# Kernel optimization log

Hardware: AMD Instinct MI355X
Metric: run time of the kernel (lower is better)

## Reference

```python
import jax, jax.numpy as jnp
import numpy as np

N = 50000      # nodes
E = 800000     # edges (before self-loops)
D = 128        # input_dim == hidden_dim
L = 3          # num_layers
EPS = 1e-5     # BatchNorm eps


def setup_inputs() -> dict:
    key = jax.random.key(0)
    k0, k1, k2 = jax.random.split(key, 3)
    x = jax.random.normal(k0, (N, D), dtype=jnp.float32)
    edge_index = jax.random.randint(k1, (2, E), 0, N, dtype=jnp.int32)
    # stacked per-layer params (layer 0 is input_dim->hidden, same shape since D==hidden)
    W = jax.random.normal(k2, (L, D, D), dtype=jnp.float32) / np.float32(np.sqrt(D))
    b = jnp.zeros((L, D), dtype=jnp.float32)
    gamma = jnp.ones((L, D), dtype=jnp.float32)
    beta = jnp.zeros((L, D), dtype=jnp.float32)
    return {"x": x, "edge_index": edge_index, "W": W, "b": b, "gamma": gamma, "beta": beta}


def reference(x, edge_index, W, b, gamma, beta):
    # --- GCN symmetric normalization with self-loops (PyG GCNConv default) ---
    loop = jnp.arange(N, dtype=edge_index.dtype)
    src = jnp.concatenate([edge_index[0], loop])      # [E+N]
    dst = jnp.concatenate([edge_index[1], loop])      # [E+N]
    deg = jax.ops.segment_sum(jnp.ones_like(dst, dtype=x.dtype), dst, num_segments=N)
    dinv = jax.lax.rsqrt(deg)                          # deg >= 1 due to self-loops
    norm = (dinv[src] * dinv[dst])[:, None]            # [E+N, 1]

    h = x
    for i in range(L):
        # GCNConv: aggregate norm * (h W)[src] into dst, then bias
        m = h @ W[i]                                   # [N, D]
        h = jax.ops.segment_sum(m[src] * norm, dst, num_segments=N) + b[i]
        # BatchNorm1d (training-mode batch statistics, biased variance)
        mu = jnp.mean(h, axis=0)
        var = jnp.var(h, axis=0)
        h = gamma[i] * (h - mu) * jax.lax.rsqrt(var + EPS) + beta[i]
        # ReLU; dropout is identity in eval mode
        h = jax.nn.relu(h)
    return h
```

## Files before the change

kernel.cpp:

```cpp
#include <hip/hip_runtime.h>
#include <hip/hip_bf16.h>

#define N_NODES 50000
#define N_EDGES 800000
#define DIM 128
#define BN_EPS 1e-5f
#define GATHER_BLOCKS (N_NODES / 4)
#define RED_BLOCKS 125
#define CAP 48

#define PART_SHIFT 7
#define PART_SIZE 128
#define NPARTS ((N_NODES + PART_SIZE - 1) / PART_SIZE)
#define QSTRIDE 32
#define BIN_EPB 2048
#define BIN_BLOCKS ((N_EDGES + BIN_EPB - 1) / BIN_EPB)
#define QCAP2 2560
#define GEMM_BLOCKS ((N_NODES + 31) / 32)

typedef __attribute__((ext_vector_type(8))) short short8;
typedef __attribute__((ext_vector_type(4))) float float4v;

__device__ __forceinline__ float bf16_bits_to_f32(unsigned short u) {
    union { unsigned int i; float f; } c;
    c.i = ((unsigned int)u) << 16;
    return c.f;
}

__device__ __forceinline__ float bf16_lo(unsigned int u) {
    union { unsigned int i; float f; } c;
    c.i = u << 16;
    return c.f;
}

__device__ __forceinline__ float bf16_hi(unsigned int u) {
    union { unsigned int i; float f; } c;
    c.i = u & 0xFFFF0000u;
    return c.f;
}

__device__ __forceinline__ unsigned short f32_to_bf16_bits(float f) {
    union { float f; unsigned int i; } c;
    c.f = f;
    unsigned int lsb = (c.i >> 16) & 1u;
    c.i += 0x7FFFu + lsb;
    return (unsigned short)(c.i >> 16);
}

__global__ __launch_bounds__(256) void zero_int(int* __restrict__ p, int n) {
    int i = blockIdx.x * blockDim.x + threadIdx.x;
    if (i < n) p[i] = 0;
}

__global__ __launch_bounds__(256) void prep(
    const unsigned short* __restrict__ xu,
    const void* __restrict__ W, const void* __restrict__ b,
    const void* __restrict__ g, const void* __restrict__ be,
    float* __restrict__ modeg, unsigned short* __restrict__ Wt,
    float* __restrict__ pf32,
    int* __restrict__ qcnt, float* __restrict__ stats, int* __restrict__ done) {
    __shared__ int okc;
    if (threadIdx.x == 0) okc = 0;
    __syncthreads();
    int ok = 0;
    for (int i = threadIdx.x; i < 512; i += 256) {
        unsigned e = (xu[i] >> 7) & 0xFFu;
        if (e >= 96u && e <= 159u) ok++;
    }
    atomicAdd(&okc, ok);
    __syncthreads();
    const bool mf32 = okc < 480;

    if (blockIdx.x == 0) {
        if (threadIdx.x == 0) { modeg[0] = mf32 ? 1.0f : 0.0f; done[0] = 0; done[1] = 0; }
        for (int i = threadIdx.x; i < NPARTS; i += 256) qcnt[(size_t)i * QSTRIDE] = 0;
        stats[threadIdx.x] = 0.0f;
    }

    int i = blockIdx.x * 256 + threadIdx.x;
    const int NW = 3 * DIM * DIM;
    if (i < NW) {
        int l = i >> 14;
        int rem = i & 16383;
        int k = rem >> 7;
        int n = rem & 127;
        unsigned short v = mf32 ? f32_to_bf16_bits(((const float*)W)[i])
                                : ((const unsigned short*)W)[i];
        Wt[(size_t)l * DIM * DIM + (size_t)n * DIM + k] = v;
    } else if (i < NW + 3 * 3 * DIM) {
        int p = i - NW;
        int which = p / 384;
        int r = p - which * 384;
        const void* srcp = (which == 0) ? b : (which == 1) ? g : be;
        float v = mf32 ? ((const float*)srcp)[r]
                       : bf16_bits_to_f32(((const unsigned short*)srcp)[r]);
        pf32[which * 384 + r] = v;
    }
}

__global__ __launch_bounds__(256) void fused_a(
    const int* __restrict__ src, const int* __restrict__ dst,
    int* __restrict__ qcnt, unsigned int* __restrict__ queue,
    const void* __restrict__ x, const unsigned short* __restrict__ Wt,
    const float* __restrict__ mode, unsigned short* __restrict__ A) {
    __shared__ int lcnt[NPARTS];
    __shared__ int loff[NPARTS];
    const int bid = blockIdx.x;
    if (bid < BIN_BLOCKS) {
        const int t = threadIdx.x;
        const int blk0 = bid * BIN_EPB;
        const int nval = min(BIN_EPB, N_EDGES - blk0);
        for (int i = t; i < NPARTS; i += 256) lcnt[i] = 0;
        __syncthreads();
        for (int li = t; li < nval; li += 256) {
            int d = dst[blk0 + li];
            if ((unsigned)d < (unsigned)N_NODES)
                atomicAdd(&lcnt[d >> PART_SHIFT], 1);
        }
        __syncthreads();
        for (int i = t; i < NPARTS; i += 256) {
            int c = lcnt[i];
            loff[i] = c ? atomicAdd(&qcnt[(size_t)i * QSTRIDE], c) : 0;
        }
        __syncthreads();
        for (int li = t; li < nval; li += 256) {
            int d = dst[blk0 + li];
            if ((unsigned)d < (unsigned)N_NODES) {
                int s = src[blk0 + li];
                int part = d >> PART_SHIFT;
                int pos = atomicAdd(&loff[part], 1);
                if (pos < QCAP2)
                    queue[(size_t)part * QCAP2 + pos] =
                        (unsigned int)(s & 0xFFFF) |
                        ((unsigned int)(d & (PART_SIZE - 1)) << 16);
            }
        }
        return;
    }
    const int wave = threadIdx.x >> 6;
    const int lane = threadIdx.x & 63;
    const int quad = lane >> 4;
    const int nidx = lane & 15;
    const int row0 = (bid - BIN_BLOCKS) * 32;
    const bool mf = mode[0] > 0.5f;

    short8 bfrag[2][4];
    #pragma unroll
    for (int half = 0; half < 2; ++half) {
        int c = wave * 32 + half * 16 + nidx;
        #pragma unroll
        for (int kk = 0; kk < 4; ++kk)
            bfrag[half][kk] = *(const short8*)(Wt + (size_t)c * DIM + kk * 32 + quad * 8);
    }

    #pragma unroll
    for (int tile = 0; tile < 2; ++tile) {
        const int rt = row0 + tile * 16;
        if (rt >= N_NODES) break;
        short8 afrag[4];
        if (mf) {
            const float* xf = (const float*)x;
            #pragma unroll
            for (int kk = 0; kk < 4; ++kk) {
                const float4v* xr = (const float4v*)(xf + (size_t)(rt + nidx) * DIM + kk * 32 + quad * 8);
                float4v p0 = xr[0], p1 = xr[1];
                #pragma unroll
                for (int j = 0; j < 4; ++j) {
                    afrag[kk][j]     = (short)f32_to_bf16_bits(p0[j]);
                    afrag[kk][4 + j] = (short)f32_to_bf16_bits(p1[j]);
                }
            }
        } else {
            const unsigned short* hu = (const unsigned short*)x;
            #pragma unroll
            for (int kk = 0; kk < 4; ++kk)
                afrag[kk] = *(const short8*)(hu + (size_t)(rt + nidx) * DIM + kk * 32 + quad * 8);
        }

        float4v acc0 = {0.f, 0.f, 0.f, 0.f};
        float4v acc1 = {0.f, 0.f, 0.f, 0.f};
        #pragma unroll
        for (int kk = 0; kk < 4; ++kk) {
            acc0 = __builtin_amdgcn_mfma_f32_16x16x32_bf16(afrag[kk], bfrag[0][kk], acc0, 0, 0, 0);
            acc1 = __builtin_amdgcn_mfma_f32_16x16x32_bf16(afrag[kk], bfrag[1][kk], acc1, 0, 0, 0);
        }

        #pragma unroll
        for (int r = 0; r < 4; ++r) {
            int row = rt + quad * 4 + r;
            size_t i0 = (size_t)row * DIM + wave * 32 + nidx;
            A[i0]      = f32_to_bf16_bits(acc0[r]);
            A[i0 + 16] = f32_to_bf16_bits(acc1[r]);
        }
    }
}

__global__ __launch_bounds__(256) void csr_build(
    const int* __restrict__ qcnt, const unsigned int* __restrict__ queue,
    unsigned short* __restrict__ colu, int* __restrict__ cnt,
    float* __restrict__ dinv) {
    __shared__ int lcnt[PART_SIZE];
    const int p = blockIdx.x;
    if (threadIdx.x < PART_SIZE) lcnt[threadIdx.x] = 0;
    __syncthreads();
    const int base = p << PART_SHIFT;
    const int n = min(qcnt[(size_t)p * QSTRIDE], QCAP2);
    const unsigned int* qp = queue + (size_t)p * QCAP2;
    for (int i = threadIdx.x; i < n; i += 256) {
        unsigned int pk = qp[i];
        int dl = (pk >> 16) & (PART_SIZE - 1);
        int s  = pk & 0xFFFFu;
        int pos = atomicAdd(&lcnt[dl], 1);
        if (pos < CAP)
            colu[(size_t)(base + dl) * CAP + pos] = (unsigned short)s;
    }
    __syncthreads();
    if (threadIdx.x < PART_SIZE) {
        int d = base + threadIdx.x;
        if (d < N_NODES) {
            int c = lcnt[threadIdx.x];
            cnt[d] = c;
            dinv[d] = rsqrtf((float)c + 1.0f);
        }
    }
}

__global__ __launch_bounds__(256) void make_dinv(const int* __restrict__ cnt,
                                                 float* __restrict__ dinv) {
    int v = blockIdx.x * blockDim.x + threadIdx.x;
    if (v < N_NODES) dinv[v] = rsqrtf((float)cnt[v] + 1.0f);
}

__global__ __launch_bounds__(256) void gemm_scale(
    const void* hsrc, int kind, int b_bf16,
    const unsigned short* __restrict__ Wt,
    const float* __restrict__ dinv,
    const float* __restrict__ mode,
    const float* __restrict__ alpha, const float* __restrict__ delta,
    unsigned short* A, float* __restrict__ B, int write_b) {
    const int wave = threadIdx.x >> 6;
    const int lane = threadIdx.x & 63;
    const int quad = lane >> 4;
    const int nidx = lane & 15;
    const int row0 = blockIdx.x * 32;
    const bool mf = mode[0] > 0.5f;

    short8 bfrag[2][4];
    #pragma unroll
    for (int half = 0; half < 2; ++half) {
        int c = wave * 32 + half * 16 + nidx;
        #pragma unroll
        for (int kk = 0; kk < 4; ++kk)
            bfrag[half][kk] = *(const short8*)(Wt + (size_t)c * DIM + kk * 32 + quad * 8);
    }

    #pragma unroll
    for (int tile = 0; tile < 2; ++tile) {
        const int rt = row0 + tile * 16;
        if (rt >= N_NODES) break;

        short8 afrag[4];
        if (kind == 0) {
            if (mf) {
                const float* xf = (const float*)hsrc;
                #pragma unroll
                for (int kk = 0; kk < 4; ++kk) {
                    const float4v* xr = (const float4v*)(xf + (size_t)(rt + nidx) * DIM + kk * 32 + quad * 8);
                    float4v p0 = xr[0], p1 = xr[1];
                    #pragma unroll
                    for (int j = 0; j < 4; ++j) {
                        afrag[kk][j]     = (short)f32_to_bf16_bits(p0[j]);
                        afrag[kk][4 + j] = (short)f32_to_bf16_bits(p1[j]);
                    }
                }
            } else {
                const unsigned short* hu = (const unsigned short*)hsrc;
                #pragma unroll
                for (int kk = 0; kk < 4; ++kk)
                    afrag[kk] = *(const short8*)(hu + (size_t)(rt + nidx) * DIM + kk * 32 + quad * 8);
            }
        } else if (b_bf16) {
            const unsigned short* Bh = (const unsigned short*)hsrc;
            const float dv = dinv[rt + nidx];
            #pragma unroll
            for (int kk = 0; kk < 4; ++kk) {
                short8 braw = *(const short8*)(Bh + (size_t)(rt + nidx) * DIM + kk * 32 + quad * 8);
                const float* ap = alpha + kk * 32 + quad * 8;
                const float* dp = delta + kk * 32 + quad * 8;
                float4v A0 = *(const float4v*)ap, A1 = *(const float4v*)(ap + 4);
                float4v D0 = *(const float4v*)dp, D1 = *(const float4v*)(dp + 4);
                #pragma unroll
                for (int j = 0; j < 4; ++j) {
                    float v0 = bf16_bits_to_f32((unsigned short)braw[j]);
                    float v1 = bf16_bits_to_f32((unsigned short)braw[4 + j]);
                    float h0 = fmaxf(fmaf(A0[j] * dv, v0, D0[j]), 0.f);
                    float h1 = fmaxf(fmaf(A1[j] * dv, v1, D1[j]), 0.f);
                    afrag[kk][j]     = (short)f32_to_bf16_bits(h0);
                    afrag[kk][4 + j] = (short)f32_to_bf16_bits(h1);
                }
            }
        } else {
            const float* Bf = (const float*)hsrc;
            const float dv = dinv[rt + nidx];
            #pragma unroll
            for (int kk = 0; kk < 4; ++kk) {
                const float* bp = Bf + (size_t)(rt + nidx) * DIM + kk * 32 + quad * 8;
                float4v p0 = *(const float4v*)bp;
                float4v p1 = *(const float4v*)(bp + 4);
                const float* ap = alpha + kk * 32 + quad * 8;
                const float* dp = delta + kk * 32 + quad * 8;
                float4v A0 = *(const float4v*)ap, A1 = *(const float4v*)(ap + 4);
                float4v D0 = *(const float4v*)dp, D1 = *(const float4v*)(dp + 4);
                #pragma unroll
                for (int j = 0; j < 4; ++j) {
                    float h0 = fmaxf(fmaf(A0[j] * dv, p0[j], D0[j]), 0.f);
                    float h1 = fmaxf(fmaf(A1[j] * dv, p1[j], D1[j]), 0.f);
                    afrag[kk][j]     = (short)f32_to_bf16_bits(h0);
                    afrag[kk][4 + j] = (short)f32_to_bf16_bits(h1);
                }
            }
        }

        float4v acc0 = {0.f, 0.f, 0.f, 0.f};
        float4v acc1 = {0.f, 0.f, 0.f, 0.f};
        #pragma unroll
        for (int kk = 0; kk < 4; ++kk) {
            acc0 = __builtin_amdgcn_mfma_f32_16x16x32_bf16(afrag[kk], bfrag[0][kk], acc0, 0, 0, 0);
            acc1 = __builtin_amdgcn_mfma_f32_16x16x32_bf16(afrag[kk], bfrag[1][kk], acc1, 0, 0, 0);
        }

        #pragma unroll
        for (int r = 0; r < 4; ++r) {
            int row = rt + quad * 4 + r;
            float d = dinv[row];
            float v0 = acc0[r] * d;
            float v1 = acc1[r] * d;
            size_t i0 = (size_t)row * DIM + wave * 32 + nidx;
            size_t i1 = i0 + 16;
            A[i0] = f32_to_bf16_bits(v0);
            A[i1] = f32_to_bf16_bits(v1);
            if (write_b) { B[i0] = v0; B[i1] = v1; }
        }
    }
}

#define FMA8(vv, ww) do { \
    a0 = fmaf(ww, bf16_lo(vv.x), a0); a1 = fmaf(ww, bf16_hi(vv.x), a1); \
    a2 = fmaf(ww, bf16_lo(vv.y), a2); a3 = fmaf(ww, bf16_hi(vv.y), a3); \
    a4 = fmaf(ww, bf16_lo(vv.z), a4); a5 = fmaf(ww, bf16_hi(vv.z), a5); \
    a6 = fmaf(ww, bf16_lo(vv.w), a6); a7 = fmaf(ww, bf16_hi(vv.w), a7); } while (0)

#define CHUNK16(jbase) do { \
    int i0 = (jbase) + g, i1 = (jbase) + 4 + g, i2 = (jbase) + 8 + g, i3 = (jbase) + 12 + g; \
    int   s0 = __shfl(cv, i0);  float w0 = __shfl(wv, i0); \
    int   s1 = __shfl(cv, i1);  float w1 = __shfl(wv, i1); \
    int   s2 = __shfl(cv, i2);  float w2 = __shfl(wv, i2); \
    int   s3 = __shfl(cv, i3);  float w3 = __shfl(wv, i3); \
    uint4 v0 = *(const uint4*)(A + (size_t)s0 * DIM + c8); \
    uint4 v1 = *(const uint4*)(A + (size_t)s1 * DIM + c8); \
    uint4 v2 = *(const uint4*)(A + (size_t)s2 * DIM + c8); \
    uint4 v3 = *(const uint4*)(A + (size_t)s3 * DIM + c8); \
    FMA8(v0, w0); FMA8(v1, w1); FMA8(v2, w2); FMA8(v3, w3); } while (0)

template <int SC>
__global__ __launch_bounds__(256) void gather_csr(
    const int* __restrict__ cnt, const unsigned short* __restrict__ colu,
    const unsigned short* __restrict__ A,
    const float* __restrict__ dinv, const float* __restrict__ bias,
    unsigned short* __restrict__ Bh, float* __restrict__ partial) {
    __shared__ float sacc[4][128], sacc2[4][128];
    const int wave = threadIdx.x >> 6;
    const int lane = threadIdx.x & 63;
    const int g    = lane >> 4;
    const int c8   = (lane & 15) * 8;
    const int node = blockIdx.x * 4 + wave;
    const int deg  = min(cnt[node], CAP);
    const int lo   = node * CAP;
    const float dv = dinv[node];

    int   cv = (lane < deg) ? (int)colu[lo + lane] : 0;
    float wv = (lane < deg) ? (SC ? dinv[cv] : 1.0f) : 0.0f;

    float a0, a1, a2, a3, a4, a5, a6, a7;
    {
        uint4 sv = *(const uint4*)(A + (size_t)node * DIM + c8);
        const float scl = (g == 0) ? (SC ? dv : 1.0f) : 0.0f;
        a0 = scl * bf16_lo(sv.x); a1 = scl * bf16_hi(sv.x);
        a2 = scl * bf16_lo(sv.y); a3 = scl * bf16_hi(sv.y);
        a4 = scl * bf16_lo(sv.z); a5 = scl * bf16_hi(sv.z);
        a6 = scl * bf16_lo(sv.w); a7 = scl * bf16_hi(sv.w);
    }

    CHUNK16(0);
    if (16 < deg) CHUNK16(16);
    if (32 < deg) CHUNK16(32);

    a0 += __shfl_xor(a0, 16); a0 += __shfl_xor(a0, 32);
    a1 += __shfl_xor(a1, 16); a1 += __shfl_xor(a1, 32);
    a2 += __shfl_xor(a2, 16); a2 += __shfl_xor(a2, 32);
    a3 += __shfl_xor(a3, 16); a3 += __shfl_xor(a3, 32);
    a4 += __shfl_xor(a4, 16); a4 += __shfl_xor(a4, 32);
    a5 += __shfl_xor(a5, 16); a5 += __shfl_xor(a5, 32);
    a6 += __shfl_xor(a6, 16); a6 += __shfl_xor(a6, 32);
    a7 += __shfl_xor(a7, 16); a7 += __shfl_xor(a7, 32);

    if (lane < 16) {
        unsigned int p0 = (unsigned int)f32_to_bf16_bits(a0) | ((unsigned int)f32_to_bf16_bits(a1) << 16);
        unsigned int p1 = (unsigned int)f32_to_bf16_bits(a2) | ((unsigned int)f32_to_bf16_bits(a3) << 16);
        unsigned int p2 = (unsigned int)f32_to_bf16_bits(a4) | ((unsigned int)f32_to_bf16_bits(a5) << 16);
        unsigned int p3 = (unsigned int)f32_to_bf16_bits(a6) | ((unsigned int)f32_to_bf16_bits(a7) << 16);
        uint4 st = {p0, p1, p2, p3};
        *(uint4*)(Bh + (size_t)node * DIM + c8) = st;
        float4 b0 = *(const float4*)(bias + c8);
        float4 b1 = *(const float4*)(bias + c8 + 4);
        float v0 = fmaf(dv, a0, b0.x), v1 = fmaf(dv, a1, b0.y);
        float v2 = fmaf(dv, a2, b0.z), v3 = fmaf(dv, a3, b0.w);
        float v4 = fmaf(dv, a4, b1.x), v5 = fmaf(dv, a5, b1.y);
        float v6 = fmaf(dv, a6, b1.z), v7 = fmaf(dv, a7, b1.w);
        sacc[wave][c8]     = v0;  sacc2[wave][c8]     = v0 * v0;
        sacc[wave][c8 + 1] = v1;  sacc2[wave][c8 + 1] = v1 * v1;
        sacc[wave][c8 + 2] = v2;  sacc2[wave][c8 + 2] = v2 * v2;
        sacc[wave][c8 + 3] = v3;  sacc2[wave][c8 + 3] = v3 * v3;
        sacc[wave][c8 + 4] = v4;  sacc2[wave][c8 + 4] = v4 * v4;
        sacc[wave][c8 + 5] = v5;  sacc2[wave][c8 + 5] = v5 * v5;
        sacc[wave][c8 + 6] = v6;  sacc2[wave][c8 + 6] = v6 * v6;
        sacc[wave][c8 + 7] = v7;  sacc2[wave][c8 + 7] = v7 * v7;
    }
    __syncthreads();
    const int t = threadIdx.x;
    float s;
    if (t < 128) s = sacc[0][t] + sacc[1][t] + sacc[2][t] + sacc[3][t];
    else { int c = t - 128; s = sacc2[0][c] + sacc2[1][c] + sacc2[2][c] + sacc2[3][c]; }
    partial[(size_t)blockIdx.x * 256 + t] = s;
}

__global__ __launch_bounds__(256) void reduce_coefs(
    const float* __restrict__ partial, float* __restrict__ stats,
    int* __restrict__ done, const float* __restrict__ pf32, int l,
    float* __restrict__ alpha, float* __restrict__ delta) {
    const int t = threadIdx.x;
    const int rows = GATHER_BLOCKS / RED_BLOCKS;
    const int r0 = blockIdx.x * rows;
    float s = 0.f;
    for (int i = 0; i < rows; ++i)
        s += partial[(size_t)(r0 + i) * 256 + t];
    atomicAdd(&stats[t], s);
    __threadfence();
    __shared__ int lastFlag;
    if (t == 0) lastFlag = (atomicAdd(done, 1) == RED_BLOCKS - 1) ? 1 : 0;
    __syncthreads();
    if (lastFlag && t < 128) {
        float cs  = atomicAdd(&stats[t], 0.0f);
        float css = atomicAdd(&stats[t + 128], 0.0f);
        const float invN = 1.0f / N_NODES;
        float mu = cs * invN;
        float var = css * invN - mu * mu;
        float istd = rsqrtf(var + BN_EPS);
        float gg = pf32[384 + l * 128 + t];
        float bt = pf32[768 + l * 128 + t];
        float bi = pf32[l * 128 + t];
        float al = gg * istd;
        alpha[t] = al;
        delta[t] = al * (bi - mu) + bt;
        atomicExch(&stats[t], 0.0f);
        atomicExch(&stats[t + 128], 0.0f);
        if (t == 0) atomicExch(done, 0);
    }
}

__global__ __launch_bounds__(128) void bn_coefs(
    const float* __restrict__ pf32, int l,
    float* __restrict__ colsum, float* __restrict__ colsumsq,
    float* __restrict__ alpha, float* __restrict__ delta) {
    int c = threadIdx.x;
    const float invN = 1.0f / N_NODES;
    float mu = colsum[c] * invN;
    float var = colsumsq[c] * invN - mu * mu;
    float istd = rsqrtf(var + BN_EPS);
    float gg = pf32[384 + l * 128 + c];
    float bt = pf32[768 + l * 128 + c];
    float bi = pf32[l * 128 + c];
    float al = gg * istd;
    alpha[c] = al;
    delta[c] = al * (bi - mu) + bt;
    colsum[c] = 0.f;
    colsumsq[c] = 0.f;
}

__global__ __launch_bounds__(256) void hist_dst(const int* __restrict__ dst,
                                                int* __restrict__ cnt) {
    int e = blockIdx.x * blockDim.x + threadIdx.x;
    if (e < N_EDGES) atomicAdd(&cnt[dst[e]], 1);
}

__global__ __launch_bounds__(256) void scatter_edges(
    const int* __restrict__ src, const int* __restrict__ dst,
    const unsigned short* __restrict__ A, float* __restrict__ B) {
    int t = blockIdx.x * blockDim.x + threadIdx.x;
    int e = t >> 4;
    if (e >= N_EDGES) return;
    int f = (t & 15) * 8;
    int s = src[e], d = dst[e];
    short8 v = *(const short8*)(A + (size_t)s * DIM + f);
    float* bp = B + (size_t)d * DIM + f;
    #pragma unroll
    for (int j = 0; j < 8; ++j)
        atomicAdd(bp + j, bf16_bits_to_f32((unsigned short)v[j]));
}

__global__ __launch_bounds__(256) void bn_reduce(
    const float* __restrict__ B, const float* __restrict__ dinv,
    const float* __restrict__ bias,
    float* __restrict__ colsum, float* __restrict__ colsumsq) {
    int c = threadIdx.x & 127;
    int half = threadIdx.x >> 7;
    float bb = bias[c];
    float s = 0.f, s2 = 0.f;
    for (int row = blockIdx.x * 2 + half; row < N_NODES; row += gridDim.x * 2) {
        float v = dinv[row] * B[(size_t)row * DIM + c] + bb;
        s += v;
        s2 += v * v;
    }
    __shared__ float ls[128], ls2[128];
    if (half == 1) { ls[c] = s; ls2[c] = s2; }
    __syncthreads();
    if (half == 0) {
        atomicAdd(&colsum[c], s + ls[c]);
        atomicAdd(&colsumsq[c], s2 + ls2[c]);
    }
}

__global__ __launch_bounds__(256) void bn_apply(
    const void* __restrict__ Bv, int b_bf16,
    const float* __restrict__ dinv,
    const float* __restrict__ alpha, const float* __restrict__ delta,
    const float* __restrict__ mode, void* __restrict__ out) {
    int t = blockIdx.x * blockDim.x + threadIdx.x;
    if (t >= N_NODES * DIM / 8) return;
    int row = t >> 4;
    int c8  = (t & 15) * 8;
    float dv = dinv[row];
    float4 A0 = *(const float4*)(alpha + c8), A1 = *(const float4*)(alpha + c8 + 4);
    float4 D0 = *(const float4*)(delta + c8), D1 = *(const float4*)(delta + c8 + 4);
    float v[8];
    if (b_bf16) {
        uint4 bv = *(const uint4*)((const unsigned short*)Bv + (size_t)row * DIM + c8);
        v[0] = bf16_lo(bv.x); v[1] = bf16_hi(bv.x);
        v[2] = bf16_lo(bv.y); v[3] = bf16_hi(bv.y);
        v[4] = bf16_lo(bv.z); v[5] = bf16_hi(bv.z);
        v[6] = bf16_lo(bv.w); v[7] = bf16_hi(bv.w);
    } else {
        const float* bf = (const float*)Bv + (size_t)row * DIM + c8;
        #pragma unroll
        for (int j = 0; j < 8; ++j) v[j] = bf[j];
    }
    float al[8] = {A0.x, A0.y, A0.z, A0.w, A1.x, A1.y, A1.z, A1.w};
    float de[8] = {D0.x, D0.y, D0.z, D0.w, D1.x, D1.y, D1.z, D1.w};
    float r[8];
    #pragma unroll
    for (int j = 0; j < 8; ++j)
        r[j] = fmaxf(fmaf(al[j] * dv, v[j], de[j]), 0.f);
    if (mode[0] > 0.5f) {
        float4* op = (float4*)((float*)out + (size_t)row * DIM + c8);
        float4 o0 = {r[0], r[1], r[2], r[3]};
        float4 o1 = {r[4], r[5], r[6], r[7]};
        op[0] = o0; op[1] = o1;
    } else {
        unsigned int p0 = (unsigned int)f32_to_bf16_bits(r[0]) | ((unsigned int)f32_to_bf16_bits(r[1]) << 16);
        unsigned int p1 = (unsigned int)f32_to_bf16_bits(r[2]) | ((unsigned int)f32_to_bf16_bits(r[3]) << 16);
        unsigned int p2 = (unsigned int)f32_to_bf16_bits(r[4]) | ((unsigned int)f32_to_bf16_bits(r[5]) << 16);
        unsigned int p3 = (unsigned int)f32_to_bf16_bits(r[6]) | ((unsigned int)f32_to_bf16_bits(r[7]) << 16);
        uint4 st = {p0, p1, p2, p3};
        *(uint4*)((unsigned short*)out + (size_t)row * DIM + c8) = st;
    }
}

extern "C" void kernel_launch(void* const* d_in, const int* in_sizes, int n_in,
                              void* d_out, int out_size, void* d_ws, size_t ws_size,
                              hipStream_t stream) {
    const void* x  = d_in[0];
    const int*  ei = (const int*)d_in[1];
    const void* W  = d_in[2];
    const void* b  = d_in[3];
    const void* g  = d_in[4];
    const void* be = d_in[5];

    unsigned short* hA = (unsigned short*)d_out;

    char* ws = (char*)d_ws;
    size_t off = 0;
    auto alloc = [&](size_t bytes) {
        char* p = ws + off;
        off = (off + bytes + 255) & ~(size_t)255;
        return p;
    };
    float* dinv     = (float*)alloc((size_t)N_NODES * 4);
    float* B        = (float*)alloc((size_t)N_NODES * DIM * 4);
    unsigned short* Wt = (unsigned short*)alloc((size_t)3 * DIM * DIM * 2);
    float* pf32     = (float*)alloc(3 * 3 * DIM * 4);
    float* stats    = (float*)alloc(256 * 4);
    float* alphaB   = (float*)alloc(128 * 4);
    float* deltaB   = (float*)alloc(128 * 4);
    float* mode     = (float*)alloc(64 * 4);
    int*   done     = (int*)alloc(64 * 4);
    int*   cnt      = (int*)alloc((size_t)N_NODES * 4);
    unsigned short* colu = (unsigned short*)alloc((size_t)N_NODES * CAP * 2);
    float* partial  = (float*)alloc((size_t)GATHER_BLOCKS * 256 * 4);
    int*   qcnt     = (int*)alloc((size_t)NPARTS * QSTRIDE * 4);
    unsigned int* queue = (unsigned int*)partial;
    const bool csr_ok = (ws_size >= off) || (ws_size == 0);
    float* colsum = stats;
    float* colsumsq = stats + 128;
    unsigned short* Bh = (unsigned short*)B;

    const int* srcv = ei;
    const int* dstv = ei + N_EDGES;

    const int PREP_BLOCKS = (3 * DIM * DIM + 3 * 3 * DIM + 255) / 256;
    prep<<<PREP_BLOCKS, 256, 0, stream>>>(
        (const unsigned short*)x, W, b, g, be, mode, Wt, pf32, qcnt, stats, done);

    if (csr_ok) {
        fused_a<<<BIN_BLOCKS + GEMM_BLOCKS, 256, 0, stream>>>(
            srcv, dstv, qcnt, queue, x, Wt, mode, hA);
        csr_build<<<NPARTS, 256, 0, stream>>>(qcnt, queue, colu, cnt, dinv);

        for (int l = 0; l < 3; ++l) {
            if (l > 0)
                gemm_scale<<<GEMM_BLOCKS, 256, 0, stream>>>(
                    (const void*)B, 2, 1, Wt + (size_t)l * DIM * DIM, dinv, mode,
                    alphaB, deltaB, hA, B, 0);
            if (l == 0)
                gather_csr<1><<<GATHER_BLOCKS, 256, 0, stream>>>(
                    cnt, colu, hA, dinv, pf32 + l * 128, Bh, partial);
            else
                gather_csr<0><<<GATHER_BLOCKS, 256, 0, stream>>>(
                    cnt, colu, hA, dinv, pf32 + l * 128, Bh, partial);
            reduce_coefs<<<RED_BLOCKS, 256, 0, stream>>>(
                partial, stats, done, pf32, l, alphaB, deltaB);
            if (l == 2)
                bn_apply<<<(N_NODES * DIM / 8 + 255) / 256, 256, 0, stream>>>(
                    (const void*)B, 1, dinv, alphaB, deltaB, mode, d_out);
        }
    } else {
        zero_int<<<(N_NODES + 255) / 256, 256, 0, stream>>>(cnt, N_NODES);
        hist_dst<<<(N_EDGES + 255) / 256, 256, 0, stream>>>(dstv, cnt);
        make_dinv<<<(N_NODES + 255) / 256, 256, 0, stream>>>(cnt, dinv);

        for (int l = 0; l < 3; ++l) {
            const void* hin = (l == 0) ? x : (const void*)B;
            gemm_scale<<<GEMM_BLOCKS, 256, 0, stream>>>(
                hin, (l == 0) ? 0 : 2, 0, Wt + (size_t)l * DIM * DIM, dinv, mode,
                alphaB, deltaB, hA, B, 1);
            scatter_edges<<<(N_EDGES * 16) / 256, 256, 0, stream>>>(srcv, dstv, hA, B);
            bn_reduce<<<256, 256, 0, stream>>>(B, dinv, pf32 + l * 128, colsum, colsumsq);
            bn_coefs<<<1, 128, 0, stream>>>(pf32, l, colsum, colsumsq, alphaB, deltaB);
            if (l == 2)
                bn_apply<<<(N_NODES * DIM / 8 + 255) / 256, 256, 0, stream>>>(
                    (const void*)B, 0, dinv, alphaB, deltaB, mode, d_out);
        }
    }
}
```

Baseline: 315.4 us.

## Gather two nodes per wave and fuse final BN reduce with apply

The CSR gather kernel now has each wave aggregate two destination nodes with interleaved chunk loads. This halves the number of blocks and puts more independent memory requests in flight per wave. For the last layer, the statistics reduction and the BatchNorm/ReLU apply are merged into one kernel. It uses a software grid barrier (atomic counter plus spin) so the separate coefficient and apply launches disappear. The trade-offs are that the barrier depends on all 391 blocks being resident at once, and that stats/done are not reset inside the new kernel, so correctness relies on them being cleared elsewhere.

```diff
diff --git a/kernel.cpp b/kernel.cpp
--- a/kernel.cpp
+++ b/kernel.cpp
@@ -5,7 +5,7 @@
 #define N_EDGES 800000
 #define DIM 128
 #define BN_EPS 1e-5f
-#define GATHER_BLOCKS (N_NODES / 4)
+#define GATHER_BLOCKS (N_NODES / 8)
 #define RED_BLOCKS 125
 #define CAP 48
 
@@ -17,6 +17,7 @@
 #define BIN_BLOCKS ((N_EDGES + BIN_EPB - 1) / BIN_EPB)
 #define QCAP2 2560
 #define GEMM_BLOCKS ((N_NODES + 31) / 32)
+#define RA_BLOCKS 391
 
 typedef __attribute__((ext_vector_type(8))) short short8;
 typedef __attribute__((ext_vector_type(4))) float float4v;
@@ -344,23 +345,26 @@
     }
 }
 
-#define FMA8(vv, ww) do { \
-    a0 = fmaf(ww, bf16_lo(vv.x), a0); a1 = fmaf(ww, bf16_hi(vv.x), a1); \
-    a2 = fmaf(ww, bf16_lo(vv.y), a2); a3 = fmaf(ww, bf16_hi(vv.y), a3); \
-    a4 = fmaf(ww, bf16_lo(vv.z), a4); a5 = fmaf(ww, bf16_hi(vv.z), a5); \
-    a6 = fmaf(ww, bf16_lo(vv.w), a6); a7 = fmaf(ww, bf16_hi(vv.w), a7); } while (0)
-
-#define CHUNK16(jbase) do { \
-    int i0 = (jbase) + g, i1 = (jbase) + 4 + g, i2 = (jbase) + 8 + g, i3 = (jbase) + 12 + g; \
-    int   s0 = __shfl(cv, i0);  float w0 = __shfl(wv, i0); \
-    int   s1 = __shfl(cv, i1);  float w1 = __shfl(wv, i1); \
-    int   s2 = __shfl(cv, i2);  float w2 = __shfl(wv, i2); \
-    int   s3 = __shfl(cv, i3);  float w3 = __shfl(wv, i3); \
-    uint4 v0 = *(const uint4*)(A + (size_t)s0 * DIM + c8); \
-    uint4 v1 = *(const uint4*)(A + (size_t)s1 * DIM + c8); \
-    uint4 v2 = *(const uint4*)(A + (size_t)s2 * DIM + c8); \
-    uint4 v3 = *(const uint4*)(A + (size_t)s3 * DIM + c8); \
-    FMA8(v0, w0); FMA8(v1, w1); FMA8(v2, w2); FMA8(v3, w3); } while (0)
+#define FMA8X(vv, ww, A0,A1,A2,A3,A4,A5,A6,A7) do { \
+    A0 = fmaf(ww, bf16_lo(vv.x), A0); A1 = fmaf(ww, bf16_hi(vv.x), A1); \
+    A2 = fmaf(ww, bf16_lo(vv.y), A2); A3 = fmaf(ww, bf16_hi(vv.y), A3); \
+    A4 = fmaf(ww, bf16_lo(vv.z), A4); A5 = fmaf(ww, bf16_hi(vv.z), A5); \
+    A6 = fmaf(ww, bf16_lo(vv.w), A6); A7 = fmaf(ww, bf16_hi(vv.w), A7); } while (0)
+
+#define CHUNK16X(jbase, cvv, wvv, A0,A1,A2,A3,A4,A5,A6,A7) do { \
+    int i0_ = (jbase) + g, i1_ = (jbase) + 4 + g, i2_ = (jbase) + 8 + g, i3_ = (jbase) + 12 + g; \
+    int   s0_ = __shfl(cvv, i0_);  float w0_ = __shfl(wvv, i0_); \
+    int   s1_ = __shfl(cvv, i1_);  float w1_ = __shfl(wvv, i1_); \
+    int   s2_ = __shfl(cvv, i2_);  float w2_ = __shfl(wvv, i2_); \
+    int   s3_ = __shfl(cvv, i3_);  float w3_ = __shfl(wvv, i3_); \
+    uint4 v0_ = *(const uint4*)(A + (size_t)s0_ * DIM + c8); \
+    uint4 v1_ = *(const uint4*)(A + (size_t)s1_ * DIM + c8); \
+    uint4 v2_ = *(const uint4*)(A + (size_t)s2_ * DIM + c8); \
+    uint4 v3_ = *(const uint4*)(A + (size_t)s3_ * DIM + c8); \
+    FMA8X(v0_, w0_, A0,A1,A2,A3,A4,A5,A6,A7); \
+    FMA8X(v1_, w1_, A0,A1,A2,A3,A4,A5,A6,A7); \
+    FMA8X(v2_, w2_, A0,A1,A2,A3,A4,A5,A6,A7); \
+    FMA8X(v3_, w3_, A0,A1,A2,A3,A4,A5,A6,A7); } while (0)
 
 template <int SC>
 __global__ __launch_bounds__(256) void gather_csr(
@@ -368,32 +372,46 @@
     const unsigned short* __restrict__ A,
     const float* __restrict__ dinv, const float* __restrict__ bias,
     unsigned short* __restrict__ Bh, float* __restrict__ partial) {
-    __shared__ float sacc[4][128], sacc2[4][128];
+    __shared__ float sacc[8][128], sacc2[8][128];
     const int wave = threadIdx.x >> 6;
     const int lane = threadIdx.x & 63;
     const int g    = lane >> 4;
     const int c8   = (lane & 15) * 8;
-    const int node = blockIdx.x * 4 + wave;
-    const int deg  = min(cnt[node], CAP);
-    const int lo   = node * CAP;
-    const float dv = dinv[node];
-
-    int   cv = (lane < deg) ? (int)colu[lo + lane] : 0;
-    float wv = (lane < deg) ? (SC ? dinv[cv] : 1.0f) : 0.0f;
+    const int n0 = blockIdx.x * 8 + wave * 2;
+    const int n1 = n0 + 1;
+    const int deg0 = min(cnt[n0], CAP);
+    const int deg1 = min(cnt[n1], CAP);
+    const int lo0 = n0 * CAP, lo1 = n1 * CAP;
+    const float dv0 = dinv[n0], dv1 = dinv[n1];
+
+    int   cv0 = (lane < deg0) ? (int)colu[lo0 + lane] : 0;
+    int   cv1 = (lane < deg1) ? (int)colu[lo1 + lane] : 0;
+    float wv0 = (lane < deg0) ? (SC ? dinv[cv0] : 1.0f) : 0.0f;
+    float wv1 = (lane < deg1) ? (SC ? dinv[cv1] : 1.0f) : 0.0f;
 
     float a0, a1, a2, a3, a4, a5, a6, a7;
+    float b0, b1, b2, b3, b4, b5, b6, b7;
     {
-        uint4 sv = *(const uint4*)(A + (size_t)node * DIM + c8);
-        const float scl = (g == 0) ? (SC ? dv : 1.0f) : 0.0f;
-        a0 = scl * bf16_lo(sv.x); a1 = scl * bf16_hi(sv.x);
-        a2 = scl * bf16_lo(sv.y); a3 = scl * bf16_hi(sv.y);
-        a4 = scl * bf16_lo(sv.z); a5 = scl * bf16_hi(sv.z);
-        a6 = scl * bf16_lo(sv.w); a7 = scl * bf16_hi(sv.w);
-    }
-
-    CHUNK16(0);
-    if (16 < deg) CHUNK16(16);
-    if (32 < deg) CHUNK16(32);
+        uint4 s0 = *(const uint4*)(A + (size_t)n0 * DIM + c8);
+        uint4 s1 = *(const uint4*)(A + (size_t)n1 * DIM + c8);
+        const float sc0 = (g == 0) ? (SC ? dv0 : 1.0f) : 0.0f;
+        const float sc1 = (g == 0) ? (SC ? dv1 : 1.0f) : 0.0f;
+        a0 = sc0 * bf16_lo(s0.x); a1 = sc0 * bf16_hi(s0.x);
+        a2 = sc0 * bf16_lo(s0.y); a3 = sc0 * bf16_hi(s0.y);
+        a4 = sc0 * bf16_lo(s0.z); a5 = sc0 * bf16_hi(s0.z);
+        a6 = sc0 * bf16_lo(s0.w); a7 = sc0 * bf16_hi(s0.w);
+        b0 = sc1 * bf16_lo(s1.x); b1 = sc1 * bf16_hi(s1.x);
+        b2 = sc1 * bf16_lo(s1.y); b3 = sc1 * bf16_hi(s1.y);
+        b4 = sc1 * bf16_lo(s1.z); b5 = sc1 * bf16_hi(s1.z);
+        b6 = sc1 * bf16_lo(s1.w); b7 = sc1 * bf16_hi(s1.w);
+    }
+
+    CHUNK16X(0, cv0, wv0, a0,a1,a2,a3,a4,a5,a6,a7);
+    CHUNK16X(0, cv1, wv1, b0,b1,b2,b3,b4,b5,b6,b7);
+    if (16 < deg0) CHUNK16X(16, cv0, wv0, a0,a1,a2,a3,a4,a5,a6,a7);
+    if (16 < deg1) CHUNK16X(16, cv1, wv1, b0,b1,b2,b3,b4,b5,b6,b7);
+    if (32 < deg0) CHUNK16X(32, cv0, wv0, a0,a1,a2,a3,a4,a5,a6,a7);
+    if (32 < deg1) CHUNK16X(32, cv1, wv1, b0,b1,b2,b3,b4,b5,b6,b7);
 
     a0 += __shfl_xor(a0, 16); a0 += __shfl_xor(a0, 32);
     a1 += __shfl_xor(a1, 16); a1 += __shfl_xor(a1, 32);
@@ -403,34 +421,71 @@
     a5 += __shfl_xor(a5, 16); a5 += __shfl_xor(a5, 32);
     a6 += __shfl_xor(a6, 16); a6 += __shfl_xor(a6, 32);
     a7 += __shfl_xor(a7, 16); a7 += __shfl_xor(a7, 32);
+    b0 += __shfl_xor(b0, 16); b0 += __shfl_xor(b0, 32);
+    b1 += __shfl_xor(b1, 16); b1 += __shfl_xor(b1, 32);
+    b2 += __shfl_xor(b2, 16); b2 += __shfl_xor(b2, 32);
+    b3 += __shfl_xor(b3, 16); b3 += __shfl_xor(b3, 32);
+    b4 += __shfl_xor(b4, 16); b4 += __shfl_xor(b4, 32);
+    b5 += __shfl_xor(b5, 16); b5 += __shfl_xor(b5, 32);
+    b6 += __shfl_xor(b6, 16); b6 += __shfl_xor(b6, 32);
+    b7 += __shfl_xor(b7, 16); b7 += __shfl_xor(b7, 32);
 
     if (lane < 16) {
-        unsigned int p0 = (unsigned int)f32_to_bf16_bits(a0) | ((unsigned int)f32_to_bf16_bits(a1) << 16);
-        unsigned int p1 = (unsigned int)f32_to_bf16_bits(a2) | ((unsigned int)f32_to_bf16_bits(a3) << 16);
-        unsigned int p2 = (unsigned int)f32_to_bf16_bits(a4) | ((unsigned int)f32_to_bf16_bits(a5) << 16);
-        unsigned int p3 = (unsigned int)f32_to_bf16_bits(a6) | ((unsigned int)f32_to_bf16_bits(a7) << 16);
-        uint4 st = {p0, p1, p2, p3};
-        *(uint4*)(Bh + (size_t)node * DIM + c8) = st;
-        float4 b0 = *(const float4*)(bias + c8);
-        float4 b1 = *(const float4*)(bias + c8 + 4);
-        float v0 = fmaf(dv, a0, b0.x), v1 = fmaf(dv, a1, b0.y);
-        float v2 = fmaf(dv, a2, b0.z), v3 = fmaf(dv, a3, b0.w);
-        float v4 = fmaf(dv, a4, b1.x), v5 = fmaf(dv, a5, b1.y);
-        float v6 = fmaf(dv, a6, b1.z), v7 = fmaf(dv, a7, b1.w);
-        sacc[wave][c8]     = v0;  sacc2[wave][c8]     = v0 * v0;
-        sacc[wave][c8 + 1] = v1;  sacc2[wave][c8 + 1] = v1 * v1;
-        sacc[wave][c8 + 2] = v2;  sacc2[wave][c8 + 2] = v2 * v2;
-        sacc[wave][c8 + 3] = v3;  sacc2[wave][c8 + 3] = v3 * v3;
-        sacc[wave][c8 + 4] = v4;  sacc2[wave][c8 + 4] = v4 * v4;
-        sacc[wave][c8 + 5] = v5;  sacc2[wave][c8 + 5] = v5 * v5;
-        sacc[wave][c8 + 6] = v6;  sacc2[wave][c8 + 6] = v6 * v6;
-        sacc[wave][c8 + 7] = v7;  sacc2[wave][c8 + 7] = v7 * v7;
+        {
+            unsigned int p0 = (unsigned int)f32_to_bf16_bits(a0) | ((unsigned int)f32_to_bf16_bits(a1) << 16);
+            unsigned int p1 = (unsigned int)f32_to_bf16_bits(a2) | ((unsigned int)f32_to_bf16_bits(a3) << 16);
+            unsigned int p2 = (unsigned int)f32_to_bf16_bits(a4) | ((unsigned int)f32_to_bf16_bits(a5) << 16);
+            unsigned int p3 = (unsigned int)f32_to_bf16_bits(a6) | ((unsigned int)f32_to_bf16_bits(a7) << 16);
+            uint4 st = {p0, p1, p2, p3};
+            *(uint4*)(Bh + (size_t)n0 * DIM + c8) = st;
+        }
+        {
+            unsigned int p0 = (unsigned int)f32_to_bf16_bits(b0) | ((unsigned int)f32_to_bf16_bits(b1) << 16);
+            unsigned int p1 = (unsigned int)f32_to_bf16_bits(b2) | ((unsigned int)f32_to_bf16_bits(b3) << 16);
+            unsigned int p2 = (unsigned int)f32_to_bf16_bits(b4) | ((unsigned int)f32_to_bf16_bits(b5) << 16);
+            unsigned int p3 = (unsigned int)f32_to_bf16_bits(b6) | ((unsigned int)f32_to_bf16_bits(b7) << 16);
+            uint4 st = {p0, p1, p2, p3};
+            *(uint4*)(Bh + (size_t)n1 * DIM + c8) = st;
+        }
+        float4 bb0 = *(const float4*)(bias + c8);
+        float4 bb1 = *(const float4*)(bias + c8 + 4);
+        float v0 = fmaf(dv0, a0, bb0.x), v1 = fmaf(dv0, a1, bb0.y);
+        float v2 = fmaf(dv0, a2, bb0.z), v3 = fmaf(dv0, a3, bb0.w);
+        float v4 = fmaf(dv0, a4, bb1.x), v5 = fmaf(dv0, a5, bb1.y);
+        float v6 = fmaf(dv0, a6, bb1.z), v7 = fmaf(dv0, a7, bb1.w);
+        float u0 = fmaf(dv1, b0, bb0.x), u1 = fmaf(dv1, b1, bb0.y);
+        float u2 = fmaf(dv1, b2, bb0.z), u3 = fmaf(dv1, b3, bb0.w);
+        float u4 = fmaf(dv1, b4, bb1.x), u5 = fmaf(dv1, b5, bb1.y);
+        float u6 = fmaf(dv1, b6, bb1.z), u7 = fmaf(dv1, b7, bb1.w);
+        const int w0i = wave * 2, w1i = wave * 2 + 1;
+        sacc[w0i][c8]     = v0;  sacc2[w0i][c8]     = v0 * v0;
+        sacc[w0i][c8 + 1] = v1;  sacc2[w0i][c8 + 1] = v1 * v1;
+        sacc[w0i][c8 + 2] = v2;  sacc2[w0i][c8 + 2] = v2 * v2;
+        sacc[w0i][c8 + 3] = v3;  sacc2[w0i][c8 + 3] = v3 * v3;
+        sacc[w0i][c8 + 4] = v4;  sacc2[w0i][c8 + 4] = v4 * v4;
+        sacc[w0i][c8 + 5] = v5;  sacc2[w0i][c8 + 5] = v5 * v5;
+        sacc[w0i][c8 + 6] = v6;  sacc2[w0i][c8 + 6] = v6 * v6;
+        sacc[w0i][c8 + 7] = v7;  sacc2[w0i][c8 + 7] = v7 * v7;
+        sacc[w1i][c8]     = u0;  sacc2[w1i][c8]     = u0 * u0;
+        sacc[w1i][c8 + 1] = u1;  sacc2[w1i][c8 + 1] = u1 * u1;
+        sacc[w1i][c8 + 2] = u2;  sacc2[w1i][c8 + 2] = u2 * u2;
+        sacc[w1i][c8 + 3] = u3;  sacc2[w1i][c8 + 3] = u3 * u3;
+        sacc[w1i][c8 + 4] = u4;  sacc2[w1i][c8 + 4] = u4 * u4;
+        sacc[w1i][c8 + 5] = u5;  sacc2[w1i][c8 + 5] = u5 * u5;
+        sacc[w1i][c8 + 6] = u6;  sacc2[w1i][c8 + 6] = u6 * u6;
+        sacc[w1i][c8 + 7] = u7;  sacc2[w1i][c8 + 7] = u7 * u7;
     }
     __syncthreads();
     const int t = threadIdx.x;
     float s;
-    if (t < 128) s = sacc[0][t] + sacc[1][t] + sacc[2][t] + sacc[3][t];
-    else { int c = t - 128; s = sacc2[0][c] + sacc2[1][c] + sacc2[2][c] + sacc2[3][c]; }
+    if (t < 128) {
+        s = sacc[0][t] + sacc[1][t] + sacc[2][t] + sacc[3][t]
+          + sacc[4][t] + sacc[5][t] + sacc[6][t] + sacc[7][t];
+    } else {
+        int c = t - 128;
+        s = sacc2[0][c] + sacc2[1][c] + sacc2[2][c] + sacc2[3][c]
+          + sacc2[4][c] + sacc2[5][c] + sacc2[6][c] + sacc2[7][c];
+    }
     partial[(size_t)blockIdx.x * 256 + t] = s;
 }
 
@@ -465,6 +520,77 @@
         atomicExch(&stats[t], 0.0f);
         atomicExch(&stats[t + 128], 0.0f);
         if (t == 0) atomicExch(done, 0);
+    }
+}
+
+__global__ __launch_bounds__(256) void reduce_apply(
+    const float* __restrict__ partial, float* __restrict__ stats,
+    int* __restrict__ done, const float* __restrict__ pf32, int l,
+    const void* __restrict__ Bv, const float* __restrict__ dinv,
+    const float* __restrict__ mode, void* __restrict__ out) {
+    const int t = threadIdx.x;
+    {
+        const int r0 = blockIdx.x * 16;
+        const int rn = min(16, GATHER_BLOCKS - r0);
+        float s = 0.f;
+        for (int i = 0; i < rn; ++i)
+            s += partial[(size_t)(r0 + i) * 256 + t];
+        atomicAdd(&stats[t], s);
+    }
+    __threadfence();
+    __syncthreads();
+    if (t == 0) {
+        atomicAdd(done, 1);
+        while (atomicAdd(done, 0) < RA_BLOCKS)
+            __builtin_amdgcn_s_sleep(8);
+    }
+    __syncthreads();
+    __threadfence();
+    __shared__ float sal[128], sde[128];
+    if (t < 128) {
+        float cs  = atomicAdd(&stats[t], 0.0f);
+        float css = atomicAdd(&stats[t + 128], 0.0f);
+        const float invN = 1.0f / N_NODES;
+        float mu = cs * invN;
+        float var = css * invN - mu * mu;
+        float istd = rsqrtf(var + BN_EPS);
+        float gg = pf32[384 + l * 128 + t];
+        float bt = pf32[768 + l * 128 + t];
+        float bi = pf32[l * 128 + t];
+        float al = gg * istd;
+        sal[t] = al;
+        sde[t] = al * (bi - mu) + bt;
+    }
+    __syncthreads();
+    const bool mf = mode[0] > 0.5f;
+    const unsigned short* Bh = (const unsigned short*)Bv;
+    for (int it = blockIdx.x * 256 + t; it < N_NODES * DIM / 8; it += RA_BLOCKS * 256) {
+        int row = it >> 4;
+        int c8  = (it & 15) * 8;
+        float dv = dinv[row];
+        uint4 bv = *(const uint4*)(Bh + (size_t)row * DIM + c8);
+        float v[8];
+        v[0] = bf16_lo(bv.x); v[1] = bf16_hi(bv.x);
+        v[2] = bf16_lo(bv.y); v[3] = bf16_hi(bv.y);
+        v[4] = bf16_lo(bv.z); v[5] = bf16_hi(bv.z);
+        v[6] = bf16_lo(bv.w); v[7] = bf16_hi(bv.w);
+        float r[8];
+        #pragma unroll
+        for (int j = 0; j < 8; ++j)
+            r[j] = fmaxf(fmaf(sal[c8 + j] * dv, v[j], sde[c8 + j]), 0.f);
+        if (mf) {
+            float4* op = (float4*)((float*)out + (size_t)row * DIM + c8);
+            float4 o0 = {r[0], r[1], r[2], r[3]};
+            float4 o1 = {r[4], r[5], r[6], r[7]};
+            op[0] = o0; op[1] = o1;
+        } else {
+            unsigned int p0 = (unsigned int)f32_to_bf16_bits(r[0]) | ((unsigned int)f32_to_bf16_bits(r[1]) << 16);
+            unsigned int p1 = (unsigned int)f32_to_bf16_bits(r[2]) | ((unsigned int)f32_to_bf16_bits(r[3]) << 16);
+            unsigned int p2 = (unsigned int)f32_to_bf16_bits(r[4]) | ((unsigned int)f32_to_bf16_bits(r[5]) << 16);
+            unsigned int p3 = (unsigned int)f32_to_bf16_bits(r[6]) | ((unsigned int)f32_to_bf16_bits(r[7]) << 16);
+            uint4 st = {p0, p1, p2, p3};
+            *(uint4*)((unsigned short*)out + (size_t)row * DIM + c8) = st;
+        }
     }
 }
 
@@ -636,11 +762,12 @@
             else
                 gather_csr<0><<<GATHER_BLOCKS, 256, 0, stream>>>(
                     cnt, colu, hA, dinv, pf32 + l * 128, Bh, partial);
-            reduce_coefs<<<RED_BLOCKS, 256, 0, stream>>>(
-                partial, stats, done, pf32, l, alphaB, deltaB);
-            if (l == 2)
-                bn_apply<<<(N_NODES * DIM / 8 + 255) / 256, 256, 0, stream>>>(
-                    (const void*)B, 1, dinv, alphaB, deltaB, mode, d_out);
+            if (l < 2)
+                reduce_coefs<<<RED_BLOCKS, 256, 0, stream>>>(
+                    partial, stats, done, pf32, l, alphaB, deltaB);
+            else
+                reduce_apply<<<RA_BLOCKS, 256, 0, stream>>>(
+                    partial, stats, done, pf32, l, (const void*)B, dinv, mode, d_out);
         }
     } else {
         zero_int<<<(N_NODES + 255) / 256, 256, 0, stream>>>(cnt, N_NODES);
```

Result: slower. 388.0 us (+23.0%).
